# Kernel optimization log

Hardware: AMD Instinct MI355X
Metric: run time of the kernel (lower is better)

## Reference

```python
import jax, jax.numpy as jnp
import numpy as np

I = 1739   # input/output feature size (num_nodes)
H = 256    # hidden size
T = 2048   # trajectory length


def gru(x_seq, h0, W_ih, W_hh, b_ih, b_hh):
    """PyTorch-convention GRU over x_seq [T, I] with h0 [H]. Returns (hs [T,H], h_T [H])."""
    x_proj = x_seq @ W_ih.T + b_ih  # [T, 3H], precompute input projections

    def step(h, xp):
        hh = h @ W_hh.T + b_hh  # [3H]
        xr, xz, xn = xp[:H], xp[H:2 * H], xp[2 * H:]
        hr, hz, hn = hh[:H], hh[H:2 * H], hh[2 * H:]
        r = jax.nn.sigmoid(xr + hr)
        z = jax.nn.sigmoid(xz + hz)
        n = jnp.tanh(xn + r * hn)
        h_new = (1.0 - z) * n + z * h
        return h_new, h_new

    h_T, hs = jax.lax.scan(step, h0, x_proj)
    return hs, h_T


def setup_inputs() -> dict:
    key = jax.random.key(0)
    ks = jax.random.split(key, 12)
    s = 1.0 / np.sqrt(H)
    inp = {
        "input_trajectory": jax.random.normal(ks[0], (1, T, I), jnp.float32),
        "target_trajectory": jax.random.normal(ks[1], (1, T, I), jnp.float32),
        "W_ih_enc": jax.random.uniform(ks[2], (3 * H, I), jnp.float32, -s, s),
        "W_hh_enc": jax.random.uniform(ks[3], (3 * H, H), jnp.float32, -s, s),
        "b_ih_enc": jax.random.uniform(ks[4], (3 * H,), jnp.float32, -s, s),
        "b_hh_enc": jax.random.uniform(ks[5], (3 * H,), jnp.float32, -s, s),
        "W_ih_dec": jax.random.uniform(ks[6], (3 * H, I), jnp.float32, -s, s),
        "W_hh_dec": jax.random.uniform(ks[7], (3 * H, H), jnp.float32, -s, s),
        "b_ih_dec": jax.random.uniform(ks[8], (3 * H,), jnp.float32, -s, s),
        "b_hh_dec": jax.random.uniform(ks[9], (3 * H,), jnp.float32, -s, s),
        "W_out": jax.random.uniform(ks[10], (I, H), jnp.float32, -s, s),
        "b_out": jax.random.uniform(ks[11], (I,), jnp.float32, -s, s),
    }
    return inp


def reference(input_trajectory, target_trajectory,
              W_ih_enc, W_hh_enc, b_ih_enc, b_hh_enc,
              W_ih_dec, W_hh_dec, b_ih_dec, b_hh_dec,
              W_out, b_out):
    x = input_trajectory[0]  # [T, I], batch=1
    h0 = jnp.zeros((H,), x.dtype)
    # Encoder: only the final hidden state is used.
    _, h_enc = gru(x, h0, W_ih_enc, W_hh_enc, b_ih_enc, b_hh_enc)
    # Decoder: loop feeds each input timestep through a 1-step GRU;
    # this is exactly a GRU over the full sequence starting from h_enc.
    hs, _ = gru(x, h_enc, W_ih_dec, W_hh_dec, b_ih_dec, b_hh_dec)  # [T, H]
    # Per-step Linear is a single batched matmul over all steps.
    preds = hs @ W_out.T + b_out  # [T, I]
    # Original cats per-step (1,1,I) tensors along dim=0 -> [T, 1, I].
    return preds[:, None, :]
```

## Files before the change

### kernel.cpp

```cpp
#include <hip/hip_runtime.h>
#include <hip/hip_fp16.h>

#define TT 2048
#define II 1739
#define HN 256
#define H3 768
#define L2E 1.44269504088896f

typedef _Float16 h2 __attribute__((ext_vector_type(2)));

__device__ __forceinline__ float fdot2(h2 a, h2 b, float c) {
#if defined(__has_builtin)
#if __has_builtin(__builtin_amdgcn_fdot2)
  return __builtin_amdgcn_fdot2(a, b, c, false);
#else
  return fmaf((float)a[0], (float)b[0], fmaf((float)a[1], (float)b[1], c));
#endif
#else
  return fmaf((float)a[0], (float)b[0], fmaf((float)a[1], (float)b[1], c));
#endif
}

__device__ __forceinline__ float fast_exp2(float x) {
#if defined(__has_builtin)
#if __has_builtin(__builtin_amdgcn_exp2f)
  return __builtin_amdgcn_exp2f(x);
#else
  return exp2f(x);
#endif
#else
  return exp2f(x);
#endif
}

__device__ __forceinline__ float fast_rcp(float x) {
#if defined(__has_builtin)
#if __has_builtin(__builtin_amdgcn_rcpf)
  return __builtin_amdgcn_rcpf(x);
#else
  return 1.f / x;
#endif
#else
  return 1.f / x;
#endif
}

template <int CTRL>
__device__ __forceinline__ float dpp_qperm(float v) {
  int r = __builtin_amdgcn_update_dpp(0, __builtin_bit_cast(int, v), CTRL, 0xF, 0xF, true);
  return __builtin_bit_cast(float, r);
}

__global__ __launch_bounds__(256) void gemm_abt(
    const float* __restrict__ A, int M, int K,
    const float* __restrict__ B, int N,
    const float* __restrict__ bias1, const float* __restrict__ bias2, int b2lim,
    float s_lo, float s_hi, int slim,
    float* __restrict__ C) {
  __shared__ float As[16][64];
  __shared__ float Bs[16][64];
  const int tid = threadIdx.x;
  const int m0 = blockIdx.y * 64, n0 = blockIdx.x * 64;
  const int lr = tid >> 2;
  const int lk = (tid & 3) * 4;
  const int cx = tid & 15, cy = tid >> 4;
  float acc[4][4] = {};

  for (int k0 = 0; k0 < K; k0 += 16) {
#pragma unroll
    for (int i = 0; i < 4; ++i) {
      int k = k0 + lk + i;
      As[lk + i][lr] = (k < K) ? A[(size_t)(m0 + lr) * K + k] : 0.f;
      int bn = n0 + lr;
      Bs[lk + i][lr] = (k < K && bn < N) ? B[(size_t)bn * K + k] : 0.f;
    }
    __syncthreads();
#pragma unroll
    for (int k = 0; k < 16; ++k) {
      float4 av = *(const float4*)&As[k][cy * 4];
      float4 bv = *(const float4*)&Bs[k][cx * 4];
      const float aa[4] = {av.x, av.y, av.z, av.w};
      const float bb[4] = {bv.x, bv.y, bv.z, bv.w};
#pragma unroll
      for (int i = 0; i < 4; ++i)
#pragma unroll
        for (int j = 0; j < 4; ++j) acc[i][j] = fmaf(aa[i], bb[j], acc[i][j]);
    }
    __syncthreads();
  }
#pragma unroll
  for (int i = 0; i < 4; ++i) {
    int m = m0 + cy * 4 + i;
#pragma unroll
    for (int j = 0; j < 4; ++j) {
      int n = n0 + cx * 4 + j;
      if (n < N) {
        float b = bias1 ? bias1[n] : 0.f;
        if (bias2 && n < b2lim) b += bias2[n];
        float s = (n < slim) ? s_lo : s_hi;
        C[(size_t)m * N + n] = (acc[i][j] + b) * s;
      }
    }
  }
}

__global__ __launch_bounds__(512) void gru_seq(
    const float* __restrict__ xp,
    const float* __restrict__ Whh,
    const float* __restrict__ bhh,
    const float* __restrict__ h0,
    float* __restrict__ hs_out,
    float* __restrict__ hT_out) {
  __shared__ __align__(16) uint hbufd[2][160];

  const int tid = threadIdx.x;
  const int lane = tid & 63;
  const int wv = tid >> 6;
  const int kc = lane & 3;
  const int q = wv * 16 + (lane >> 2);
  const int u0 = 2 * q;

  h2 wreg[6][32];
#pragma unroll
  for (int uu = 0; uu < 2; ++uu) {
#pragma unroll
    for (int gg = 0; gg < 3; ++gg) {
      const float sc = (gg == 2) ? (2.f * L2E) : L2E;
      const float* wr = Whh + (size_t)(u0 + uu + gg * HN) * HN + kc * 64;
#pragma unroll
      for (int p = 0; p < 32; ++p) {
        float2 f = *(const float2*)(wr + 2 * p);
        wreg[uu * 3 + gg][p] = h2{(_Float16)(f.x * sc), (_Float16)(f.y * sc)};
      }
    }
  }

  float hj0 = h0 ? h0[u0] : 0.f;
  float hj1 = h0 ? h0[u0 + 1] : 0.f;
  const float bhn0 = bhh[2 * HN + u0] * (2.f * L2E);
  const float bhn1 = bhh[2 * HN + u0 + 1] * (2.f * L2E);

  if (tid < 128) {
    float a = h0 ? h0[2 * tid] : 0.f;
    float b = h0 ? h0[2 * tid + 1] : 0.f;
    h2 pv = h2{(_Float16)a, (_Float16)b};
    hbufd[0][(tid >> 5) * 40 + (tid & 31)] = __builtin_bit_cast(uint, pv);
  }
  __syncthreads();

  const float* xpt = xp + u0;
  const int wadr = (q >> 5) * 40 + (q & 31);

  for (int t = 0; t < TT; ++t) {
    float2 xr = *(const float2*)(xpt);
    float2 xz = *(const float2*)(xpt + HN);
    float2 xn = *(const float2*)(xpt + 2 * HN);
    xpt += H3;

    const uint* hb = &hbufd[t & 1][kc * 40];
    float a[6] = {0.f, 0.f, 0.f, 0.f, 0.f, 0.f};
#pragma unroll
    for (int qq = 0; qq < 8; ++qq) {
      uint4 v = *(const uint4*)&hb[qq * 4];
      uint hwv[4] = {v.x, v.y, v.z, v.w};
#pragma unroll
      for (int i = 0; i < 6; ++i)
#pragma unroll
        for (int p = 0; p < 4; ++p)
          a[i] = fdot2(wreg[i][qq * 4 + p], __builtin_bit_cast(h2, hwv[p]), a[i]);
    }

#pragma unroll
    for (int i = 0; i < 6; ++i) {
      float v = a[i];
      v += dpp_qperm<0xB1>(v);
      v += dpp_qperm<0x4E>(v);
      a[i] = v;
    }

    float r0 = fast_rcp(1.f + fast_exp2(-(xr.x + a[0])));
    float z0 = fast_rcp(1.f + fast_exp2(-(xz.x + a[1])));
    float n0 = fmaf(2.f, fast_rcp(1.f + fast_exp2(-fmaf(r0, a[2] + bhn0, xn.x))), -1.f);
    hj0 = fmaf(z0, hj0 - n0, n0);
    float r1 = fast_rcp(1.f + fast_exp2(-(xr.y + a[3])));
    float z1 = fast_rcp(1.f + fast_exp2(-(xz.y + a[4])));
    float n1 = fmaf(2.f, fast_rcp(1.f + fast_exp2(-fmaf(r1, a[5] + bhn1, xn.y))), -1.f);
    hj1 = fmaf(z1, hj1 - n1, n1);

    h2 pv = h2{(_Float16)hj0, (_Float16)hj1};
    if (kc == 0) {
      hbufd[(t & 1) ^ 1][wadr] = __builtin_bit_cast(uint, pv);
      if (hs_out) *(float2*)&hs_out[(size_t)t * HN + u0] = make_float2(hj0, hj1);
    }
    __syncthreads();
  }
  if (hT_out && kc == 0) *(float2*)&hT_out[u0] = make_float2(hj0, hj1);
}

extern "C" void kernel_launch(void* const* d_in, const int* in_sizes, int n_in,
                              void* d_out, int out_size, void* d_ws, size_t ws_size,
                              hipStream_t stream) {
  const float* x     = (const float*)d_in[0];
  const float* Wih_e = (const float*)d_in[2];
  const float* Whh_e = (const float*)d_in[3];
  const float* bih_e = (const float*)d_in[4];
  const float* bhh_e = (const float*)d_in[5];
  const float* Wih_d = (const float*)d_in[6];
  const float* Whh_d = (const float*)d_in[7];
  const float* bih_d = (const float*)d_in[8];
  const float* bhh_d = (const float*)d_in[9];
  const float* Wout  = (const float*)d_in[10];
  const float* bout  = (const float*)d_in[11];
  float* out = (float*)d_out;

  float* ws = (float*)d_ws;
  float* xpe  = ws;
  float* xpd  = xpe + (size_t)TT * H3;
  float* hs   = xpd + (size_t)TT * H3;
  float* henc = hs + (size_t)TT * HN;

  dim3 blk(256);
  gemm_abt<<<dim3(12, 32), blk, 0, stream>>>(x, TT, II, Wih_e, H3, bih_e, bhh_e, 2 * HN,
                                             L2E, 2.f * L2E, 2 * HN, xpe);
  gemm_abt<<<dim3(12, 32), blk, 0, stream>>>(x, TT, II, Wih_d, H3, bih_d, bhh_d, 2 * HN,
                                             L2E, 2.f * L2E, 2 * HN, xpd);
  gru_seq<<<1, 512, 0, stream>>>(xpe, Whh_e, bhh_e, nullptr, nullptr, henc);
  gru_seq<<<1, 512, 0, stream>>>(xpd, Whh_d, bhh_d, henc, hs, nullptr);
  gemm_abt<<<dim3(28, 32), blk, 0, stream>>>(hs, TT, HN, Wout, II, bout, nullptr, 0,
                                             1.f, 1.f, 0, out);
}
```

Measured before the change: 5.026 ms.

## Overlap GRU scans with input and output projection GEMMs in fused kernels

Block 0 of a fused launch runs the encoder GRU scan while the other blocks compute the decoder input projection GEMM. A second fused launch runs the decoder scan in block 0, which publishes per-64-step progress flags. The remaining blocks pull output-GEMM row tiles from an atomic job counter and spin until the matching rows of hs are ready. This hides GEMM time behind the serial recurrences, at the cost of possible CU contention with the scan block. It also wastes work, since the upper 256 threads of each 512-thread GEMM block redundantly repeat the tile, and it relies on block 0 being resident while the other blocks spin.

```diff
diff --git a/kernel.cpp b/kernel.cpp
--- a/kernel.cpp
+++ b/kernel.cpp
@@ -49,6 +49,58 @@
 __device__ __forceinline__ float dpp_qperm(float v) {
   int r = __builtin_amdgcn_update_dpp(0, __builtin_bit_cast(int, v), CTRL, 0xF, 0xF, true);
   return __builtin_bit_cast(float, r);
+}
+
+__device__ __forceinline__ void gemm_tile(
+    int tid, int bx, int by,
+    const float* __restrict__ A, int M, int K,
+    const float* __restrict__ B, int N,
+    const float* __restrict__ bias1, const float* __restrict__ bias2, int b2lim,
+    float s_lo, float s_hi, int slim,
+    float* __restrict__ C,
+    float (*As)[64], float (*Bs)[64]) {
+  const int m0 = by * 64, n0 = bx * 64;
+  const int lr = tid >> 2;
+  const int lk = (tid & 3) * 4;
+  const int cx = tid & 15, cy = tid >> 4;
+  float acc[4][4] = {};
+
+  for (int k0 = 0; k0 < K; k0 += 16) {
+#pragma unroll
+    for (int i = 0; i < 4; ++i) {
+      int k = k0 + lk + i;
+      As[lk + i][lr] = (k < K) ? A[(size_t)(m0 + lr) * K + k] : 0.f;
+      int bn = n0 + lr;
+      Bs[lk + i][lr] = (k < K && bn < N) ? B[(size_t)bn * K + k] : 0.f;
+    }
+    __syncthreads();
+#pragma unroll
+    for (int k = 0; k < 16; ++k) {
+      float4 av = *(const float4*)&As[k][cy * 4];
+      float4 bv = *(const float4*)&Bs[k][cx * 4];
+      const float aa[4] = {av.x, av.y, av.z, av.w};
+      const float bb[4] = {bv.x, bv.y, bv.z, bv.w};
+#pragma unroll
+      for (int i = 0; i < 4; ++i)
+#pragma unroll
+        for (int j = 0; j < 4; ++j) acc[i][j] = fmaf(aa[i], bb[j], acc[i][j]);
+    }
+    __syncthreads();
+  }
+#pragma unroll
+  for (int i = 0; i < 4; ++i) {
+    int m = m0 + cy * 4 + i;
+#pragma unroll
+    for (int j = 0; j < 4; ++j) {
+      int n = n0 + cx * 4 + j;
+      if (n < N) {
+        float b = bias1 ? bias1[n] : 0.f;
+        if (bias2 && n < b2lim) b += bias2[n];
+        float s = (n < slim) ? s_lo : s_hi;
+        C[(size_t)m * N + n] = (acc[i][j] + b) * s;
+      }
+    }
+  }
 }
 
 __global__ __launch_bounds__(256) void gemm_abt(
@@ -59,58 +111,18 @@
     float* __restrict__ C) {
   __shared__ float As[16][64];
   __shared__ float Bs[16][64];
-  const int tid = threadIdx.x;
-  const int m0 = blockIdx.y * 64, n0 = blockIdx.x * 64;
-  const int lr = tid >> 2;
-  const int lk = (tid & 3) * 4;
-  const int cx = tid & 15, cy = tid >> 4;
-  float acc[4][4] = {};
-
-  for (int k0 = 0; k0 < K; k0 += 16) {
-#pragma unroll
-    for (int i = 0; i < 4; ++i) {
-      int k = k0 + lk + i;
-      As[lk + i][lr] = (k < K) ? A[(size_t)(m0 + lr) * K + k] : 0.f;
-      int bn = n0 + lr;
-      Bs[lk + i][lr] = (k < K && bn < N) ? B[(size_t)bn * K + k] : 0.f;
-    }
-    __syncthreads();
-#pragma unroll
-    for (int k = 0; k < 16; ++k) {
-      float4 av = *(const float4*)&As[k][cy * 4];
-      float4 bv = *(const float4*)&Bs[k][cx * 4];
-      const float aa[4] = {av.x, av.y, av.z, av.w};
-      const float bb[4] = {bv.x, bv.y, bv.z, bv.w};
-#pragma unroll
-      for (int i = 0; i < 4; ++i)
-#pragma unroll
-        for (int j = 0; j < 4; ++j) acc[i][j] = fmaf(aa[i], bb[j], acc[i][j]);
-    }
-    __syncthreads();
-  }
-#pragma unroll
-  for (int i = 0; i < 4; ++i) {
-    int m = m0 + cy * 4 + i;
-#pragma unroll
-    for (int j = 0; j < 4; ++j) {
-      int n = n0 + cx * 4 + j;
-      if (n < N) {
-        float b = bias1 ? bias1[n] : 0.f;
-        if (bias2 && n < b2lim) b += bias2[n];
-        float s = (n < slim) ? s_lo : s_hi;
-        C[(size_t)m * N + n] = (acc[i][j] + b) * s;
-      }
-    }
-  }
-}
-
-__global__ __launch_bounds__(512) void gru_seq(
+  gemm_tile(threadIdx.x, blockIdx.x, blockIdx.y, A, M, K, B, N,
+            bias1, bias2, b2lim, s_lo, s_hi, slim, C, As, Bs);
+}
+
+__device__ void gru_scan(
     const float* __restrict__ xp,
     const float* __restrict__ Whh,
     const float* __restrict__ bhh,
     const float* __restrict__ h0,
     float* __restrict__ hs_out,
-    float* __restrict__ hT_out) {
+    float* __restrict__ hT_out,
+    unsigned int* __restrict__ prog) {
   __shared__ __align__(16) uint hbufd[2][160];
 
   const int tid = threadIdx.x;
@@ -148,14 +160,16 @@
   }
   __syncthreads();
 
-  const float* xpt = xp + u0;
   const int wadr = (q >> 5) * 40 + (q & 31);
 
   for (int t = 0; t < TT; ++t) {
-    float2 xr = *(const float2*)(xpt);
-    float2 xz = *(const float2*)(xpt + HN);
-    float2 xn = *(const float2*)(xpt + 2 * HN);
-    xpt += H3;
+    float2 xr, xz, xn;
+    {
+      const float* xpt = xp + (size_t)t * H3 + u0;
+      xr = *(const float2*)(xpt);
+      xz = *(const float2*)(xpt + HN);
+      xn = *(const float2*)(xpt + 2 * HN);
+    }
 
     const uint* hb = &hbufd[t & 1][kc * 40];
     float a[6] = {0.f, 0.f, 0.f, 0.f, 0.f, 0.f};
@@ -193,8 +207,63 @@
       if (hs_out) *(float2*)&hs_out[(size_t)t * HN + u0] = make_float2(hj0, hj1);
     }
     __syncthreads();
+    if (prog && (t & 63) == 63 && tid == 0) {
+      __hip_atomic_store(&prog[t >> 6], 1u, __ATOMIC_RELEASE,
+                         __HIP_MEMORY_SCOPE_AGENT);
+    }
   }
   if (hT_out && kc == 0) *(float2*)&hT_out[u0] = make_float2(hj0, hj1);
+}
+
+__global__ __launch_bounds__(512) void fused_enc(
+    const float* __restrict__ xpe, const float* __restrict__ Whh_e,
+    const float* __restrict__ bhh_e, float* __restrict__ henc,
+    const float* __restrict__ x, const float* __restrict__ Wih_d,
+    const float* __restrict__ bih_d, const float* __restrict__ bhh_d,
+    float* __restrict__ xpd) {
+  if (blockIdx.x == 0) {
+    gru_scan(xpe, Whh_e, bhh_e, nullptr, nullptr, henc, nullptr);
+  } else {
+    __shared__ float As[16][64];
+    __shared__ float Bs[16][64];
+    const int b = blockIdx.x - 1;
+    gemm_tile(threadIdx.x & 255, b % 12, b / 12, x, TT, II, Wih_d, H3,
+              bih_d, bhh_d, 2 * HN, L2E, 2.f * L2E, 2 * HN, xpd, As, Bs);
+  }
+}
+
+#define NJOBS (28 * 32)
+__global__ __launch_bounds__(512) void fused_dec(
+    const float* __restrict__ xpd, const float* __restrict__ Whh_d,
+    const float* __restrict__ bhh_d, const float* __restrict__ henc,
+    float* __restrict__ hs, unsigned int* __restrict__ prog,
+    int* __restrict__ jobctr,
+    const float* __restrict__ Wout, const float* __restrict__ bout,
+    float* __restrict__ out) {
+  if (blockIdx.x == 0) {
+    gru_scan(xpd, Whh_d, bhh_d, henc, hs, nullptr, prog);
+  } else {
+    __shared__ float As[16][64];
+    __shared__ float Bs[16][64];
+    __shared__ int sjob;
+    const int tid = threadIdx.x;
+    for (;;) {
+      if (tid == 0) sjob = atomicAdd(jobctr, 1);
+      __syncthreads();
+      const int job = sjob;
+      __syncthreads();
+      if (job >= NJOBS) break;
+      const int by = job / 28, bx = job % 28;
+      if (tid == 0) {
+        while (__hip_atomic_load(&prog[by], __ATOMIC_ACQUIRE,
+                                 __HIP_MEMORY_SCOPE_AGENT) == 0u)
+          __builtin_amdgcn_s_sleep(8);
+      }
+      __syncthreads();
+      gemm_tile(tid & 255, bx, by, hs, TT, HN, Wout, II, bout, nullptr, 0,
+                1.f, 1.f, 0, out, As, Bs);
+    }
+  }
 }
 
 extern "C" void kernel_launch(void* const* d_in, const int* in_sizes, int n_in,
@@ -218,14 +287,17 @@
   float* xpd  = xpe + (size_t)TT * H3;
   float* hs   = xpd + (size_t)TT * H3;
   float* henc = hs + (size_t)TT * HN;
+  unsigned int* prog = (unsigned int*)(henc + HN);
+  int* jobctr = (int*)(prog + 32);
+
+  hipMemsetAsync(prog, 0, 64 * sizeof(unsigned int), stream);
 
   dim3 blk(256);
   gemm_abt<<<dim3(12, 32), blk, 0, stream>>>(x, TT, II, Wih_e, H3, bih_e, bhh_e, 2 * HN,
                                              L2E, 2.f * L2E, 2 * HN, xpe);
-  gemm_abt<<<dim3(12, 32), blk, 0, stream>>>(x, TT, II, Wih_d, H3, bih_d, bhh_d, 2 * HN,
-                                             L2E, 2.f * L2E, 2 * HN, xpd);
-  gru_seq<<<1, 512, 0, stream>>>(xpe, Whh_e, bhh_e, nullptr, nullptr, henc);
-  gru_seq<<<1, 512, 0, stream>>>(xpd, Whh_d, bhh_d, henc, hs, nullptr);
-  gemm_abt<<<dim3(28, 32), blk, 0, stream>>>(hs, TT, HN, Wout, II, bout, nullptr, 0,
-                                             1.f, 1.f, 0, out);
-}
+  fused_enc<<<dim3(385), dim3(512), 0, stream>>>(xpe, Whh_e, bhh_e, henc,
+                                                 x, Wih_d, bih_d, bhh_d, xpd);
+  fused_dec<<<dim3(201), dim3(512), 0, stream>>>(xpd, Whh_d, bhh_d, henc,
+                                                 hs, prog, jobctr,
+                                                 Wout, bout, out);
+}
```

After: 5.733 ms. 14.1% more time.

## Replace FP32 SIMT GEMMs with FP16 MFMA GEMMs using pre-converted padded weights

Applied to the files above, without the earlier changes.

Adds a prep kernel that converts the input-projection and output weights to FP16, padding K to a multiple of 32. All three projection GEMMs are replaced by a kernel using 16x16x32 f16 MFMA instructions, converting activations to FP16 on load. This targets the FP32 scalar FMA cost of the large projection GEMMs, which run alongside the long sequential GRU kernels. It adds a per-call weight conversion pass and lowers input precision to FP16 with FP32 accumulation.

```diff
diff --git a/kernel.cpp b/kernel.cpp
--- a/kernel.cpp
+++ b/kernel.cpp
@@ -3,11 +3,14 @@
 
 #define TT 2048
 #define II 1739
+#define IIP 1760
 #define HN 256
 #define H3 768
 #define L2E 1.44269504088896f
 
 typedef _Float16 h2 __attribute__((ext_vector_type(2)));
+typedef _Float16 h8 __attribute__((ext_vector_type(8)));
+typedef float f4 __attribute__((ext_vector_type(4)));
 
 __device__ __forceinline__ float fdot2(h2 a, h2 b, float c) {
 #if defined(__has_builtin)
@@ -51,55 +54,99 @@
   return __builtin_bit_cast(float, r);
 }
 
-__global__ __launch_bounds__(256) void gemm_abt(
-    const float* __restrict__ A, int M, int K,
-    const float* __restrict__ B, int N,
+__device__ __forceinline__ h8 h8zero() {
+  h8 v;
+#pragma unroll
+  for (int j = 0; j < 8; ++j) v[j] = (_Float16)0.f;
+  return v;
+}
+
+#define WSEG (768 * IIP)
+#define OSEG (II * HN)
+__global__ __launch_bounds__(256) void prep_f16(
+    const float* __restrict__ We, const float* __restrict__ Wd,
+    const float* __restrict__ Wo,
+    _Float16* __restrict__ weh, _Float16* __restrict__ wdh,
+    _Float16* __restrict__ woh) {
+  const int total = 2 * WSEG + OSEG;
+  for (int i = blockIdx.x * 256 + threadIdx.x; i < total; i += gridDim.x * 256) {
+    if (i < WSEG) {
+      int r = i / IIP, k = i - r * IIP;
+      weh[i] = (k < II) ? (_Float16)We[(size_t)r * II + k] : (_Float16)0.f;
+    } else if (i < 2 * WSEG) {
+      int j = i - WSEG;
+      int r = j / IIP, k = j - r * IIP;
+      wdh[j] = (k < II) ? (_Float16)Wd[(size_t)r * II + k] : (_Float16)0.f;
+    } else {
+      int j = i - 2 * WSEG;
+      woh[j] = (_Float16)Wo[j];
+    }
+  }
+}
+
+__global__ __launch_bounds__(256) void gemm16(
+    const float* __restrict__ A, int K,
+    const _Float16* __restrict__ B16, int N, int Kp,
     const float* __restrict__ bias1, const float* __restrict__ bias2, int b2lim,
     float s_lo, float s_hi, int slim,
     float* __restrict__ C) {
-  __shared__ float As[16][64];
-  __shared__ float Bs[16][64];
+  __shared__ _Float16 As[64][40];
+  __shared__ _Float16 Bs[64][40];
   const int tid = threadIdx.x;
+  const int w = tid >> 6, lane = tid & 63;
+  const int col = lane & 15, kg = lane >> 4;
   const int m0 = blockIdx.y * 64, n0 = blockIdx.x * 64;
-  const int lr = tid >> 2;
-  const int lk = (tid & 3) * 4;
-  const int cx = tid & 15, cy = tid >> 4;
-  float acc[4][4] = {};
-
-  for (int k0 = 0; k0 < K; k0 += 16) {
-#pragma unroll
-    for (int i = 0; i < 4; ++i) {
-      int k = k0 + lk + i;
-      As[lk + i][lr] = (k < K) ? A[(size_t)(m0 + lr) * K + k] : 0.f;
-      int bn = n0 + lr;
-      Bs[lk + i][lr] = (k < K && bn < N) ? B[(size_t)bn * K + k] : 0.f;
+  const int srow = tid >> 2, skq = tid & 3;
+  f4 acc[4];
+#pragma unroll
+  for (int m = 0; m < 4; ++m) acc[m] = f4{0.f, 0.f, 0.f, 0.f};
+
+  for (int k0 = 0; k0 < Kp; k0 += 32) {
+    const int kk = k0 + skq * 8;
+    h8 av = h8zero(), bv = h8zero();
+    {
+      const float* ap = A + (size_t)(m0 + srow) * K + kk;
+      if (kk + 8 <= K) {
+        float4 f0, f1;
+        __builtin_memcpy(&f0, ap, 16);
+        __builtin_memcpy(&f1, ap + 4, 16);
+        av[0] = (_Float16)f0.x; av[1] = (_Float16)f0.y;
+        av[2] = (_Float16)f0.z; av[3] = (_Float16)f0.w;
+        av[4] = (_Float16)f1.x; av[5] = (_Float16)f1.y;
+        av[6] = (_Float16)f1.z; av[7] = (_Float16)f1.w;
+      } else if (kk < K) {
+#pragma unroll
+        for (int j = 0; j < 8; ++j)
+          if (kk + j < K) av[j] = (_Float16)ap[j];
+      }
+    }
+    {
+      const int bn = n0 + srow;
+      if (bn < N) bv = *(const h8*)(B16 + (size_t)bn * Kp + kk);
     }
     __syncthreads();
-#pragma unroll
-    for (int k = 0; k < 16; ++k) {
-      float4 av = *(const float4*)&As[k][cy * 4];
-      float4 bv = *(const float4*)&Bs[k][cx * 4];
-      const float aa[4] = {av.x, av.y, av.z, av.w};
-      const float bb[4] = {bv.x, bv.y, bv.z, bv.w};
-#pragma unroll
-      for (int i = 0; i < 4; ++i)
-#pragma unroll
-        for (int j = 0; j < 4; ++j) acc[i][j] = fmaf(aa[i], bb[j], acc[i][j]);
-    }
+    *(h8*)&As[srow][skq * 8] = av;
+    *(h8*)&Bs[srow][skq * 8] = bv;
     __syncthreads();
-  }
-#pragma unroll
-  for (int i = 0; i < 4; ++i) {
-    int m = m0 + cy * 4 + i;
-#pragma unroll
-    for (int j = 0; j < 4; ++j) {
-      int n = n0 + cx * 4 + j;
-      if (n < N) {
-        float b = bias1 ? bias1[n] : 0.f;
-        if (bias2 && n < b2lim) b += bias2[n];
-        float s = (n < slim) ? s_lo : s_hi;
-        C[(size_t)m * N + n] = (acc[i][j] + b) * s;
-      }
+    h8 b = *(const h8*)&Bs[w * 16 + col][kg * 8];
+#pragma unroll
+    for (int m = 0; m < 4; ++m) {
+      h8 a = *(const h8*)&As[m * 16 + col][kg * 8];
+      acc[m] = __builtin_amdgcn_mfma_f32_16x16x32_f16(a, b, acc[m], 0, 0, 0);
+    }
+  }
+
+  const int n = n0 + w * 16 + col;
+  if (n < N) {
+    float bb = bias1[n];
+    if (bias2 && n < b2lim) bb += bias2[n];
+    const float s = (n < slim) ? s_lo : s_hi;
+#pragma unroll
+    for (int m = 0; m < 4; ++m) {
+      const int mr = m0 + m * 16 + kg * 4;
+#pragma unroll
+      for (int r = 0; r < 4; ++r)
+        C[(size_t)(mr + r) * N + n] = (acc[m][r] + bb) * s;
     }
   }
 }
@@ -148,14 +195,16 @@
   }
   __syncthreads();
 
-  const float* xpt = xp + u0;
   const int wadr = (q >> 5) * 40 + (q & 31);
 
   for (int t = 0; t < TT; ++t) {
-    float2 xr = *(const float2*)(xpt);
-    float2 xz = *(const float2*)(xpt + HN);
-    float2 xn = *(const float2*)(xpt + 2 * HN);
-    xpt += H3;
+    float2 xr, xz, xn;
+    {
+      const float* xpt = xp + (size_t)t * H3 + u0;
+      xr = *(const float2*)(xpt);
+      xz = *(const float2*)(xpt + HN);
+      xn = *(const float2*)(xpt + 2 * HN);
+    }
 
     const uint* hb = &hbufd[t & 1][kc * 40];
     float a[6] = {0.f, 0.f, 0.f, 0.f, 0.f, 0.f};
@@ -218,14 +267,18 @@
   float* xpd  = xpe + (size_t)TT * H3;
   float* hs   = xpd + (size_t)TT * H3;
   float* henc = hs + (size_t)TT * HN;
-
-  dim3 blk(256);
-  gemm_abt<<<dim3(12, 32), blk, 0, stream>>>(x, TT, II, Wih_e, H3, bih_e, bhh_e, 2 * HN,
-                                             L2E, 2.f * L2E, 2 * HN, xpe);
-  gemm_abt<<<dim3(12, 32), blk, 0, stream>>>(x, TT, II, Wih_d, H3, bih_d, bhh_d, 2 * HN,
-                                             L2E, 2.f * L2E, 2 * HN, xpd);
+  _Float16* weh = (_Float16*)(henc + HN);
+  _Float16* wdh = weh + (size_t)768 * IIP;
+  _Float16* woh = wdh + (size_t)768 * IIP;
+
+  prep_f16<<<dim3(1024), dim3(256), 0, stream>>>(Wih_e, Wih_d, Wout,
+                                                 weh, wdh, woh);
+  gemm16<<<dim3(12, 32), dim3(256), 0, stream>>>(x, II, weh, H3, IIP,
+      bih_e, bhh_e, 2 * HN, L2E, 2.f * L2E, 2 * HN, xpe);
+  gemm16<<<dim3(12, 32), dim3(256), 0, stream>>>(x, II, wdh, H3, IIP,
+      bih_d, bhh_d, 2 * HN, L2E, 2.f * L2E, 2 * HN, xpd);
   gru_seq<<<1, 512, 0, stream>>>(xpe, Whh_e, bhh_e, nullptr, nullptr, henc);
   gru_seq<<<1, 512, 0, stream>>>(xpd, Whh_d, bhh_d, henc, hs, nullptr);
-  gemm_abt<<<dim3(28, 32), blk, 0, stream>>>(hs, TT, HN, Wout, II, bout, nullptr, 0,
-                                             1.f, 1.f, 0, out);
-}
+  gemm16<<<dim3(28, 32), dim3(256), 0, stream>>>(hs, HN, woh, II, HN,
+      bout, nullptr, 0, 1.f, 1.f, 0, out);
+}
```

Result: faster. 4.598 ms (-8.5%).
